# Performance work log

Hardware: AMD Instinct MI355X
Metric: run time of the kernel (lower is better)

The kernel has to match this reference:

```python
import jax, jax.numpy as jnp
import numpy as np

N, IN_F, OUT_F, H = 8192, 256, 64, 4
NEG_SLOPE = 0.2


def setup_inputs() -> dict:
    key = jax.random.key(0)
    ks = jax.random.split(key, 8)
    inputs = jax.random.normal(ks[0], (N, IN_F), dtype=jnp.float32)
    # sparse-ish binary adjacency with self loops (sparse.softmax only sees nonzeros)
    adj = (jax.random.uniform(ks[1], (N, N)) < 0.05).astype(jnp.float32)
    idx = jnp.arange(N)
    adj = adj.at[idx, idx].set(1.0)
    stdv = 1.0 / np.sqrt(H * OUT_F)
    weight = jax.random.uniform(ks[2], (IN_F, H * OUT_F), minval=-stdv, maxval=stdv, dtype=jnp.float32)
    bias = jax.random.uniform(ks[3], (1, H * OUT_F), minval=-stdv, maxval=stdv, dtype=jnp.float32)
    # weight_u/v: stdv = 1/sqrt(size(-1)=1) = 1
    weight_u = jax.random.uniform(ks[4], (H, OUT_F, 1), minval=-1.0, maxval=1.0, dtype=jnp.float32)
    weight_v = jax.random.uniform(ks[5], (H, OUT_F, 1), minval=-1.0, maxval=1.0, dtype=jnp.float32)
    stdp = 1.0 / np.sqrt(IN_F)
    proj_w = jax.random.uniform(ks[6], (H * OUT_F, IN_F), minval=-stdp, maxval=stdp, dtype=jnp.float32)
    proj_b = jax.random.uniform(ks[7], (H * OUT_F,), minval=-stdp, maxval=stdp, dtype=jnp.float32)
    return {"inputs": inputs, "adj_mat": adj, "weight": weight, "weight_u": weight_u,
            "weight_v": weight_v, "bias": bias, "proj_w": proj_w, "proj_b": proj_b}


def reference(inputs, adj_mat, weight, weight_u, weight_v, bias, proj_w, proj_b):
    n = inputs.shape[0]
    support = (inputs @ weight).reshape(n, H, OUT_F).transpose(1, 0, 2)  # [H,N,O]
    f1 = jnp.einsum('hno,ho->hn', support, weight_u[..., 0])  # [H,N]
    f2 = jnp.einsum('hno,ho->hn', support, weight_v[..., 0])  # [H,N]
    logits = f1[:, None, :] + f2[:, :, None]                  # [H,N,N]
    w = jax.nn.leaky_relu(logits, NEG_SLOPE)
    masked = w * adj_mat                                      # adj broadcast over heads
    mask = adj_mat != 0.0
    # sparse.softmax over dim 2: softmax restricted to nonzero (edge) positions
    neg = jnp.where(mask, masked, -jnp.inf)
    m = jnp.max(neg, axis=2, keepdims=True)
    m = jnp.where(jnp.isfinite(m), m, 0.0)
    e = jnp.where(mask, jnp.exp(neg - m), 0.0)
    denom = jnp.sum(e, axis=2, keepdims=True)
    attn = e / jnp.where(denom > 0, denom, 1.0)               # [H,N,N]
    out = jnp.einsum('hnm,hmo->hno', attn, support)           # [H,N,O]
    out = out.transpose(1, 0, 2).reshape(n, H * OUT_F)
    out = out + bias
    out = out + inputs @ proj_w.T + proj_b
    return out
```

## Files before the change

### kernel.cpp

```cpp
#include <hip/hip_runtime.h>
#include <hip/hip_bf16.h>

#define N_NODES 8192
#define IN_FEAT 256
#define OUT_F   64
#define NHEAD   4
#define HF      256
#define NEG     0.2f

typedef unsigned short u16;
typedef unsigned char  u8;
typedef unsigned int   u32;
typedef unsigned long long u64;
typedef _Float16 h2    __attribute__((ext_vector_type(2)));
typedef _Float16 half8 __attribute__((ext_vector_type(8)));
typedef __attribute__((ext_vector_type(4))) float f32x4;

__global__ __launch_bounds__(256) void k_pre(const float* __restrict__ inp,
                                             const float* __restrict__ W,
                                             const float* __restrict__ PW,
                                             _Float16* __restrict__ X16,
                                             _Float16* __restrict__ W16B,
                                             float* __restrict__ anum,
                                             float* __restrict__ aden) {
    const int i = blockIdx.x * 256 + threadIdx.x;
    const float4 v = ((const float4*)inp)[i];
    union { _Float16 hh[4]; u64 q; } cv;
    cv.hh[0] = (_Float16)v.x; cv.hh[1] = (_Float16)v.y;
    cv.hh[2] = (_Float16)v.z; cv.hh[3] = (_Float16)v.w;
    ((u64*)X16)[i] = cv.q;
    ((float4*)anum)[i] = (float4){0.f, 0.f, 0.f, 0.f};
    if (i < 8192) ((float4*)aden)[i] = (float4){0.f, 0.f, 0.f, 0.f};

    if (i < 16384) {
        const int ks = i >> 11;
        const int T  = (i >> 6) & 31;
        const int lane = i & 63;
        const int q  = lane >> 4, cc = lane & 15;
        const int n  = T * 16 + cc;
        const int k0 = ks * 32 + q * 8;
        union { _Float16 hh[8]; half8 v8; } o;
        #pragma unroll
        for (int e = 0; e < 8; ++e) {
            const int k = k0 + e;
            const float s = (n < 256) ? W[k * 256 + n]
                                      : PW[(size_t)(n - 256) * 256 + k];
            o.hh[e] = (_Float16)s;
        }
        *(half8*)(W16B + (size_t)i * 8) = o.v8;
    }
}

#define GROWS 16
__global__ __launch_bounds__(256) void k_gemm(
    const _Float16* __restrict__ X16,
    const _Float16* __restrict__ W16B,
    const float* __restrict__ U,
    const float* __restrict__ V,
    const float* __restrict__ Bias,
    const float* __restrict__ PB,
    _Float16* __restrict__ suppB,
    float* __restrict__ f1,
    float* __restrict__ f2,
    float* __restrict__ outp)
{
    __shared__ __align__(16) _Float16 xl[GROWS][264];
    const int n0  = blockIdx.x * GROWS;
    const int tid = threadIdx.x;
    const int wv  = tid >> 6, lane = tid & 63;
    const int col = lane & 15, quad = lane >> 4;

    {
        const int r = tid >> 4, seg = tid & 15;
        const half8* src = (const half8*)(X16 + (size_t)(n0 + r) * 256 + seg * 16);
        *(half8*)&xl[r][seg * 16]     = src[0];
        *(half8*)&xl[r][seg * 16 + 8] = src[1];
    }
    __syncthreads();

    f32x4 acc[8];
    #pragma unroll
    for (int t = 0; t < 8; ++t) acc[t] = (f32x4){0.f, 0.f, 0.f, 0.f};

    const int qo = quad * 8;
    #pragma unroll
    for (int ks = 0; ks < 8; ++ks) {
        const half8 af = *(const half8*)&xl[col][ks * 32 + qo];
        const _Float16* bb = W16B + ((size_t)(ks * 32 + wv * 8) * 64 + lane) * 8;
        #pragma unroll
        for (int t = 0; t < 8; ++t) {
            const half8 bw = *(const half8*)(bb + (size_t)t * 512);
            acc[t] = __builtin_amdgcn_mfma_f32_16x16x32_f16(af, bw, acc[t], 0, 0, 0);
        }
    }

    if (wv < 2) {
        const int jbg  = n0 >> 5;
        const int nlo  = n0 & 31;
        const int jq   = nlo + quad * 4;
        const int e0   = jq & 7;
        const int wrow = (jq >> 3) << 4;
        #pragma unroll
        for (int t = 0; t < 8; ++t) {
            const int cg = wv * 128 + t * 16 + col;
            const int h  = cg >> 6;
            const int tp = (cg >> 4) & 3;
            union { _Float16 hh[4]; u64 q; } pk;
            #pragma unroll
            for (int reg = 0; reg < 4; ++reg) pk.hh[reg] = (_Float16)acc[t][reg];
            const size_t word = ((size_t)(h * 256 + jbg) * 4 + tp) * 64 + wrow + col;
            *(u64*)(suppB + word * 8 + e0) = pk.q;
        }
        float s1a[4] = {0,0,0,0}, s2a[4] = {0,0,0,0};
        float s1b[4] = {0,0,0,0}, s2b[4] = {0,0,0,0};
        #pragma unroll
        for (int t = 0; t < 8; ++t) {
            const int cg = wv * 128 + t * 16 + col;
            const float uu = U[cg], vv = V[cg];
            #pragma unroll
            for (int reg = 0; reg < 4; ++reg) {
                if (t < 4) { s1a[reg] += acc[t][reg] * uu; s2a[reg] += acc[t][reg] * vv; }
                else       { s1b[reg] += acc[t][reg] * uu; s2b[reg] += acc[t][reg] * vv; }
            }
        }
        #pragma unroll
        for (int m = 1; m < 16; m <<= 1) {
            #pragma unroll
            for (int reg = 0; reg < 4; ++reg) {
                s1a[reg] += __shfl_xor(s1a[reg], m);
                s2a[reg] += __shfl_xor(s2a[reg], m);
                s1b[reg] += __shfl_xor(s1b[reg], m);
                s2b[reg] += __shfl_xor(s2b[reg], m);
            }
        }
        if (col == 0) {
            const int hA = wv * 2, hB = wv * 2 + 1;
            #pragma unroll
            for (int reg = 0; reg < 4; ++reg) {
                const int n = n0 + quad * 4 + reg;
                f1[hA * N_NODES + n] = s1a[reg];
                f2[hA * N_NODES + n] = s2a[reg];
                f1[hB * N_NODES + n] = s1b[reg];
                f2[hB * N_NODES + n] = s2b[reg];
            }
        }
    } else {
        #pragma unroll
        for (int t = 0; t < 8; ++t) {
            const int cg = (wv - 2) * 128 + t * 16 + col;
            const float bb2 = Bias[cg] + PB[cg];
            #pragma unroll
            for (int reg = 0; reg < 4; ++reg) {
                const int irow = quad * 4 + reg;
                outp[(size_t)(n0 + irow) * HF + cg] = acc[t][reg] + bb2;
            }
        }
    }
}

__global__ __launch_bounds__(256) void k_prep(const float* __restrict__ f1,
                                              float* __restrict__ f1max,
                                              _Float16* __restrict__ EA16,
                                              _Float16* __restrict__ EB16) {
    __shared__ float red[256];
    const int h = blockIdx.x;
    float m = -1e30f;
    for (int j = threadIdx.x; j < N_NODES; j += 256)
        m = fmaxf(m, f1[h * N_NODES + j]);
    red[threadIdx.x] = m;
    __syncthreads();
    for (int s = 128; s > 0; s >>= 1) {
        if (threadIdx.x < s) red[threadIdx.x] = fmaxf(red[threadIdx.x], red[threadIdx.x + s]);
        __syncthreads();
    }
    const float fm = red[0];
    if (threadIdx.x == 0) f1max[h] = fm;
    for (int j = threadIdx.x; j < N_NODES; j += 256) {
        const float d = f1[h * N_NODES + j] - fm;
        EA16[(size_t)h * N_NODES + j] = (_Float16)__expf(d);
        EB16[(size_t)h * N_NODES + j] = (_Float16)__expf(NEG * d);
    }
}

#define TI 64
#define NSUB 4
#define JSPLIT_G 4
#define JW (N_NODES / JSPLIT_G)

__global__ __launch_bounds__(256, 3) void k_attn_mfma(
    const float* __restrict__ adj,
    const _Float16* __restrict__ suppB,
    const _Float16* __restrict__ EA16,
    const _Float16* __restrict__ EB16,
    const float* __restrict__ f2,
    const float* __restrict__ f1max,
    float* __restrict__ anum,
    float* __restrict__ aden)
{
    __shared__ __align__(16) _Float16 ea_lds[NHEAD][JW];
    __shared__ __align__(16) _Float16 eb_lds[NHEAD][JW];
    __shared__ __align__(4)  u8 abyte[TI][260];

    const int itile = blockIdx.x >> 2;
    const int jwin  = blockIdx.x & 3;
    const int i0    = itile * TI;
    const int J0    = jwin * JW;
    const int wv    = threadIdx.x >> 6;
    const int lane  = threadIdx.x & 63;
    const int col   = lane & 15;
    const int quad  = lane >> 4;

    {
        const _Float16* gea = EA16 + (size_t)wv * N_NODES + J0;
        const _Float16* geb = EB16 + (size_t)wv * N_NODES + J0;
        #pragma unroll
        for (int it = 0; it < 4; ++it) {
            const int off = it * 512 + lane * 8;
            *(float4*)&ea_lds[wv][off] = *(const float4*)(gea + off);
            *(float4*)&eb_lds[wv][off] = *(const float4*)(geb + off);
        }
    }
    #pragma unroll 2
    for (int rr = 0; rr < 16; ++rr) {
        const int r = (wv << 4) + rr;
        const float* ar = adj + (size_t)(i0 + r) * N_NODES + J0 + lane * 32;
        unsigned wrd = 0;
        #pragma unroll
        for (int p = 0; p < 8; ++p) {
            const float4 a = *(const float4*)(ar + p * 4);
            const unsigned nib =
                (unsigned)(a.x != 0.f)        | ((unsigned)(a.y != 0.f) << 1) |
                ((unsigned)(a.z != 0.f) << 2) | ((unsigned)(a.w != 0.f) << 3);
            wrd |= nib << (p * 4);
        }
        *(unsigned*)&abyte[r][lane * 4] = wrd;
    }
    __syncthreads();

    const int h = wv;
    const float fm = f1max[h];
    h2 caH[NSUB], cbH[NSUB];
    float ls[NSUB];
    #pragma unroll
    for (int s = 0; s < NSUB; ++s) {
        const float f2i = f2[(size_t)h * N_NODES + i0 + s * 16 + col];
        const float g  = fm + f2i;
        const float mi = fmaxf(g, NEG * g);
        const _Float16 ca = (_Float16)__expf(g - mi);
        const _Float16 cb = (_Float16)__expf(NEG * g - mi);
        caH[s][0] = ca; caH[s][1] = ca;
        cbH[s][0] = cb; cbH[s][1] = cb;
        ls[s] = 0.f;
    }
    const h2 ones = {(_Float16)1.0f, (_Float16)1.0f};

    const _Float16* sb = suppB + (size_t)h * 524288
                       + (size_t)(J0 >> 5) * 2048 + lane * 8;

    f32x4 acc[NSUB][4];
    #pragma unroll
    for (int s = 0; s < NSUB; ++s)
        #pragma unroll
        for (int t = 0; t < 4; ++t)
            acc[s][t] = (f32x4){0.f, 0.f, 0.f, 0.f};

    const int qo = quad << 3;

    #pragma unroll 2
    for (int jb = 0; jb < JW; jb += 32) {
        const int jl = jb + qo;
        const _Float16* fp = sb + (size_t)(jb >> 5) * 2048;
        const half8 bv0 = *(const half8*)(fp);
        const half8 bv1 = *(const half8*)(fp + 512);
        const half8 bv2 = *(const half8*)(fp + 1024);
        const half8 bv3 = *(const half8*)(fp + 1536);

        union { half8 v; h2 pr[4]; } ea, eb;
        ea.v = *(const half8*)&ea_lds[h][jl];
        eb.v = *(const half8*)&eb_lds[h][jl];
        const int wo = (jb >> 3) + quad;

        #pragma unroll
        for (int s = 0; s < NSUB; ++s) {
            const unsigned gw = abyte[col + s * 16][wo];
            union { half8 v; unsigned w[4]; h2 pr[4]; } af;
            #pragma unroll
            for (int p = 0; p < 4; ++p) {
                const h2 pa = ea.pr[p] * caH[s];
                const h2 pb = eb.pr[p] * cbH[s];
                const h2 x  = __builtin_elementwise_max(pa, pb);
                const unsigned mlo = (unsigned)((int)(gw << (31 - 2 * p)) >> 31) & 0x0000FFFFu;
                const unsigned mhi = (unsigned)((int)(gw << (30 - 2 * p)) >> 31) & 0xFFFF0000u;
                union { h2 hh; unsigned u; } xu;
                xu.hh = x;
                xu.u &= (mlo | mhi);
                af.w[p] = xu.u;
                ls[s] = __builtin_amdgcn_fdot2(xu.hh, ones, ls[s], false);
            }
            acc[s][0] = __builtin_amdgcn_mfma_f32_16x16x32_f16(af.v, bv0, acc[s][0], 0, 0, 0);
            acc[s][1] = __builtin_amdgcn_mfma_f32_16x16x32_f16(af.v, bv1, acc[s][1], 0, 0, 0);
            acc[s][2] = __builtin_amdgcn_mfma_f32_16x16x32_f16(af.v, bv2, acc[s][2], 0, 0, 0);
            acc[s][3] = __builtin_amdgcn_mfma_f32_16x16x32_f16(af.v, bv3, acc[s][3], 0, 0, 0);
        }
    }

    #pragma unroll
    for (int s = 0; s < NSUB; ++s) {
        ls[s] += __shfl_xor(ls[s], 16);
        ls[s] += __shfl_xor(ls[s], 32);
    }
    if (quad == 0) {
        #pragma unroll
        for (int s = 0; s < NSUB; ++s)
            unsafeAtomicAdd(aden + (size_t)h * N_NODES + i0 + s * 16 + col, ls[s]);
    }

    #pragma unroll
    for (int s = 0; s < NSUB; ++s) {
        #pragma unroll
        for (int reg = 0; reg < 4; ++reg) {
            const int irow = (quad << 2) + reg;
            float* ap = anum + (size_t)(i0 + s * 16 + irow) * HF + (h << 6) + col;
            #pragma unroll
            for (int t = 0; t < 4; ++t)
                unsafeAtomicAdd(ap + (t << 4), acc[s][t][reg]);
        }
    }
}

__global__ __launch_bounds__(256) void k_fin(const float* __restrict__ anum,
                                             const float* __restrict__ aden,
                                             float* __restrict__ out) {
    const int c = threadIdx.x;
    const int h = c >> 6;
    #pragma unroll
    for (int rr = 0; rr < 4; ++rr) {
        const int n = blockIdx.x * 4 + rr;
        out[(size_t)n * HF + c] += anum[(size_t)n * HF + c]
                                 / aden[(size_t)h * N_NODES + n];
    }
}

extern "C" void kernel_launch(void* const* d_in, const int* in_sizes, int n_in,
                              void* d_out, int out_size, void* d_ws, size_t ws_size,
                              hipStream_t stream) {
    const float* inp  = (const float*)d_in[0];
    const float* adj  = (const float*)d_in[1];
    const float* W    = (const float*)d_in[2];
    const float* U    = (const float*)d_in[3];
    const float* V    = (const float*)d_in[4];
    const float* Bias = (const float*)d_in[5];
    const float* PW   = (const float*)d_in[6];
    const float* PB   = (const float*)d_in[7];
    float* out = (float*)d_out;

    char* ws = (char*)d_ws;
    _Float16* suppB = (_Float16*)(ws);
    float* f1    = (float*)(ws + (4u << 20));
    float* f2    = (float*)(ws + (4u << 20) + (128u << 10));
    float* f1mx  = (float*)(ws + (4u << 20) + (256u << 10));
    _Float16* EA16 = (_Float16*)(ws + (4u << 20) + (576u << 10));
    _Float16* EB16 = (_Float16*)(ws + (4u << 20) + (704u << 10));
    float* aden  = (float*)(ws + (4u << 20) + (832u << 10));
    _Float16* X16  = (_Float16*)(ws + (16u << 20));
    _Float16* W16B = (_Float16*)(ws + (20u << 20));
    float* anum  = (float*)(ws + (24u << 20));

    k_pre  <<<2048, 256, 0, stream>>>(inp, W, PW, X16, W16B, anum, aden);
    k_gemm <<< 512, 256, 0, stream>>>(X16, W16B, U, V, Bias, PB,
                                      suppB, f1, f2, out);
    k_prep <<<NHEAD, 256, 0, stream>>>(f1, f1mx, EA16, EB16);
    k_attn_mfma<<<(N_NODES / TI) * JSPLIT_G, 256, 0, stream>>>(
        adj, suppB, EA16, EB16, f2, f1mx, anum, aden);
    k_fin  <<<N_NODES / 4, 256, 0, stream>>>(anum, aden, out);
}
```

Baseline: 469.5 us.

## Fuse input conversion into GEMM, double attention j-split, read exp tables from global

The input fp16 conversion and the zeroing of the accumulators move out of the pre-kernel and into the GEMM kernel, leaving only a small weight-pack kernel. This removes a separate pass over the inputs. The attention kernel now splits the j dimension 8 ways instead of 4 and drops the EA/EB LDS staging in favour of direct global loads. That shrinks LDS use, which allows 4 blocks per CU and more parallelism. In exchange there are more atomic partial-sum contributions and repeated global reads of the exp tables, which rely on cache hits.

```diff
diff --git a/kernel.cpp b/kernel.cpp
--- a/kernel.cpp
+++ b/kernel.cpp
@@ -16,44 +16,30 @@
 typedef _Float16 half8 __attribute__((ext_vector_type(8)));
 typedef __attribute__((ext_vector_type(4))) float f32x4;
 
-__global__ __launch_bounds__(256) void k_pre(const float* __restrict__ inp,
-                                             const float* __restrict__ W,
-                                             const float* __restrict__ PW,
-                                             _Float16* __restrict__ X16,
-                                             _Float16* __restrict__ W16B,
-                                             float* __restrict__ anum,
-                                             float* __restrict__ aden) {
+__global__ __launch_bounds__(256) void k_wpack(const float* __restrict__ W,
+                                               const float* __restrict__ PW,
+                                               _Float16* __restrict__ W16B) {
     const int i = blockIdx.x * 256 + threadIdx.x;
-    const float4 v = ((const float4*)inp)[i];
-    union { _Float16 hh[4]; u64 q; } cv;
-    cv.hh[0] = (_Float16)v.x; cv.hh[1] = (_Float16)v.y;
-    cv.hh[2] = (_Float16)v.z; cv.hh[3] = (_Float16)v.w;
-    ((u64*)X16)[i] = cv.q;
-    ((float4*)anum)[i] = (float4){0.f, 0.f, 0.f, 0.f};
-    if (i < 8192) ((float4*)aden)[i] = (float4){0.f, 0.f, 0.f, 0.f};
-
-    if (i < 16384) {
-        const int ks = i >> 11;
-        const int T  = (i >> 6) & 31;
-        const int lane = i & 63;
-        const int q  = lane >> 4, cc = lane & 15;
-        const int n  = T * 16 + cc;
-        const int k0 = ks * 32 + q * 8;
-        union { _Float16 hh[8]; half8 v8; } o;
-        #pragma unroll
-        for (int e = 0; e < 8; ++e) {
-            const int k = k0 + e;
-            const float s = (n < 256) ? W[k * 256 + n]
-                                      : PW[(size_t)(n - 256) * 256 + k];
-            o.hh[e] = (_Float16)s;
-        }
-        *(half8*)(W16B + (size_t)i * 8) = o.v8;
-    }
+    const int ks = i >> 11;
+    const int T  = (i >> 6) & 31;
+    const int lane = i & 63;
+    const int q  = lane >> 4, cc = lane & 15;
+    const int n  = T * 16 + cc;
+    const int k0 = ks * 32 + q * 8;
+    union { _Float16 hh[8]; half8 v8; } o;
+    #pragma unroll
+    for (int e = 0; e < 8; ++e) {
+        const int k = k0 + e;
+        const float s = (n < 256) ? W[k * 256 + n]
+                                  : PW[(size_t)(n - 256) * 256 + k];
+        o.hh[e] = (_Float16)s;
+    }
+    *(half8*)(W16B + (size_t)i * 8) = o.v8;
 }
 
 #define GROWS 16
 __global__ __launch_bounds__(256) void k_gemm(
-    const _Float16* __restrict__ X16,
+    const float* __restrict__ inp,
     const _Float16* __restrict__ W16B,
     const float* __restrict__ U,
     const float* __restrict__ V,
@@ -62,7 +48,9 @@
     _Float16* __restrict__ suppB,
     float* __restrict__ f1,
     float* __restrict__ f2,
-    float* __restrict__ outp)
+    float* __restrict__ outp,
+    float* __restrict__ anum,
+    float* __restrict__ aden)
 {
     __shared__ __align__(16) _Float16 xl[GROWS][264];
     const int n0  = blockIdx.x * GROWS;
@@ -72,9 +60,22 @@
 
     {
         const int r = tid >> 4, seg = tid & 15;
-        const half8* src = (const half8*)(X16 + (size_t)(n0 + r) * 256 + seg * 16);
-        *(half8*)&xl[r][seg * 16]     = src[0];
-        *(half8*)&xl[r][seg * 16 + 8] = src[1];
+        const float* src = inp + (size_t)(n0 + r) * 256 + seg * 16;
+        const float4 v0 = *(const float4*)(src);
+        const float4 v1 = *(const float4*)(src + 4);
+        const float4 v2 = *(const float4*)(src + 8);
+        const float4 v3 = *(const float4*)(src + 12);
+        union { _Float16 hh[8]; half8 v; } c0, c1;
+        c0.hh[0] = (_Float16)v0.x; c0.hh[1] = (_Float16)v0.y;
+        c0.hh[2] = (_Float16)v0.z; c0.hh[3] = (_Float16)v0.w;
+        c0.hh[4] = (_Float16)v1.x; c0.hh[5] = (_Float16)v1.y;
+        c0.hh[6] = (_Float16)v1.z; c0.hh[7] = (_Float16)v1.w;
+        c1.hh[0] = (_Float16)v2.x; c1.hh[1] = (_Float16)v2.y;
+        c1.hh[2] = (_Float16)v2.z; c1.hh[3] = (_Float16)v2.w;
+        c1.hh[4] = (_Float16)v3.x; c1.hh[5] = (_Float16)v3.y;
+        c1.hh[6] = (_Float16)v3.z; c1.hh[7] = (_Float16)v3.w;
+        *(half8*)&xl[r][seg * 16]     = c0.v;
+        *(half8*)&xl[r][seg * 16 + 8] = c1.v;
     }
     __syncthreads();
 
@@ -155,6 +156,14 @@
                 outp[(size_t)(n0 + irow) * HF + cg] = acc[t][reg] + bb2;
             }
         }
+    }
+
+    {
+        const float4 z = {0.f, 0.f, 0.f, 0.f};
+        float4* an = (float4*)(anum + (size_t)(n0 + (tid >> 4)) * HF + (tid & 15) * 16);
+        an[0] = z; an[1] = z; an[2] = z; an[3] = z;
+        if (tid < 64)
+            aden[(size_t)(tid >> 4) * N_NODES + n0 + (tid & 15)] = 0.f;
     }
 }
 
@@ -184,10 +193,11 @@
 
 #define TI 64
 #define NSUB 4
-#define JSPLIT_G 4
+#define JSPLIT_G 8
 #define JW (N_NODES / JSPLIT_G)
-
-__global__ __launch_bounds__(256, 3) void k_attn_mfma(
+#define ABW 132
+
+__global__ __launch_bounds__(256, 4) void k_attn_mfma(
     const float* __restrict__ adj,
     const _Float16* __restrict__ suppB,
     const _Float16* __restrict__ EA16,
@@ -197,12 +207,10 @@
     float* __restrict__ anum,
     float* __restrict__ aden)
 {
-    __shared__ __align__(16) _Float16 ea_lds[NHEAD][JW];
-    __shared__ __align__(16) _Float16 eb_lds[NHEAD][JW];
-    __shared__ __align__(4)  u8 abyte[TI][260];
-
-    const int itile = blockIdx.x >> 2;
-    const int jwin  = blockIdx.x & 3;
+    __shared__ __align__(4) u8 abyte[TI][ABW];
+
+    const int itile = blockIdx.x >> 3;
+    const int jwin  = blockIdx.x & 7;
     const int i0    = itile * TI;
     const int J0    = jwin * JW;
     const int wv    = threadIdx.x >> 6;
@@ -210,20 +218,11 @@
     const int col   = lane & 15;
     const int quad  = lane >> 4;
 
-    {
-        const _Float16* gea = EA16 + (size_t)wv * N_NODES + J0;
-        const _Float16* geb = EB16 + (size_t)wv * N_NODES + J0;
-        #pragma unroll
-        for (int it = 0; it < 4; ++it) {
-            const int off = it * 512 + lane * 8;
-            *(float4*)&ea_lds[wv][off] = *(const float4*)(gea + off);
-            *(float4*)&eb_lds[wv][off] = *(const float4*)(geb + off);
-        }
-    }
-    #pragma unroll 2
-    for (int rr = 0; rr < 16; ++rr) {
-        const int r = (wv << 4) + rr;
-        const float* ar = adj + (size_t)(i0 + r) * N_NODES + J0 + lane * 32;
+    #pragma unroll
+    for (int pass = 0; pass < 8; ++pass) {
+        const int r = (wv << 4) + pass * 2 + (lane >> 5);
+        const int w = lane & 31;
+        const float* ar = adj + (size_t)(i0 + r) * N_NODES + J0 + w * 32;
         unsigned wrd = 0;
         #pragma unroll
         for (int p = 0; p < 8; ++p) {
@@ -233,7 +232,7 @@
                 ((unsigned)(a.z != 0.f) << 2) | ((unsigned)(a.w != 0.f) << 3);
             wrd |= nib << (p * 4);
         }
-        *(unsigned*)&abyte[r][lane * 4] = wrd;
+        *(unsigned*)&abyte[r][w * 4] = wrd;
     }
     __syncthreads();
 
@@ -254,8 +253,10 @@
     }
     const h2 ones = {(_Float16)1.0f, (_Float16)1.0f};
 
-    const _Float16* sb = suppB + (size_t)h * 524288
-                       + (size_t)(J0 >> 5) * 2048 + lane * 8;
+    const _Float16* gea = EA16 + (size_t)h * N_NODES + J0;
+    const _Float16* geb = EB16 + (size_t)h * N_NODES + J0;
+    const _Float16* sb  = suppB + (size_t)h * 524288
+                        + (size_t)(J0 >> 5) * 2048 + lane * 8;
 
     f32x4 acc[NSUB][4];
     #pragma unroll
@@ -276,8 +277,8 @@
         const half8 bv3 = *(const half8*)(fp + 1536);
 
         union { half8 v; h2 pr[4]; } ea, eb;
-        ea.v = *(const half8*)&ea_lds[h][jl];
-        eb.v = *(const half8*)&eb_lds[h][jl];
+        ea.v = *(const half8*)(gea + jl);
+        eb.v = *(const half8*)(geb + jl);
         const int wo = (jb >> 3) + quad;
 
         #pragma unroll
@@ -362,13 +363,12 @@
     _Float16* EA16 = (_Float16*)(ws + (4u << 20) + (576u << 10));
     _Float16* EB16 = (_Float16*)(ws + (4u << 20) + (704u << 10));
     float* aden  = (float*)(ws + (4u << 20) + (832u << 10));
-    _Float16* X16  = (_Float16*)(ws + (16u << 20));
     _Float16* W16B = (_Float16*)(ws + (20u << 20));
     float* anum  = (float*)(ws + (24u << 20));
 
-    k_pre  <<<2048, 256, 0, stream>>>(inp, W, PW, X16, W16B, anum, aden);
-    k_gemm <<< 512, 256, 0, stream>>>(X16, W16B, U, V, Bias, PB,
-                                      suppB, f1, f2, out);
+    k_wpack<<<  64, 256, 0, stream>>>(W, PW, W16B);
+    k_gemm <<< 512, 256, 0, stream>>>(inp, W16B, U, V, Bias, PB,
+                                      suppB, f1, f2, out, anum, aden);
     k_prep <<<NHEAD, 256, 0, stream>>>(f1, f1mx, EA16, EB16);
     k_attn_mfma<<<(N_NODES / TI) * JSPLIT_G, 256, 0, stream>>>(
         adj, suppB, EA16, EB16, f2, f1mx, anum, aden);
```

New measurement: 454.2 us. 1.03x faster.
